# Optimization experiments

Hardware: AMD Instinct MI355X
Metric: run time of the kernel (lower is better)

The kernel has to match this reference:

```python
import jax, jax.numpy as jnp
import numpy as np

CH = 128
C2 = CH // 2
TEMP = 5.0
RATE = 2  # down conv: k=2,s=2,p=0 ; up: convtranspose k=2,s=2,p=0


def _down(x, w, b):
    # Conv2d(ch, ch, kernel=2, stride=2, pad=0) as a patch contraction
    B, C, H, W = x.shape
    xr = x.reshape(B, C, H // 2, 2, W // 2, 2)
    return jnp.einsum('bcipjq,ocpq->boij', xr, w) + b[None, :, None, None]


def _conv1x1(x, w):
    # w: [out, in]
    return jnp.einsum('bchw,oc->bohw', x, w)


def _maxpool2(x):
    B, C, H, W = x.shape
    return x.reshape(B, C, H // 2, 2, W // 2, 2).max(axis=(3, 5))


def _up(x, w, b):
    # ConvTranspose2d(ch, ch, kernel=2, stride=2, pad=0): each pixel -> 2x2 block
    # w: [in, out, 2, 2] (PyTorch layout)
    B, C, H, W = x.shape
    y = jnp.einsum('bchw,copq->bohpwq', x, w).reshape(B, w.shape[1], H * 2, W * 2)
    return y + b[None, :, None, None]


def setup_inputs() -> dict:
    key = jax.random.key(0)
    ks = jax.random.split(key, 12)
    B, H, W = 4, 192, 192
    sc = 0.05
    return {
        'input_x': jax.random.normal(ks[0], (B, CH, H, W), jnp.float32),
        'input_y': jax.random.normal(ks[1], (B, CH, H, W), jnp.float32),
        'down0_w': jax.random.normal(ks[2], (CH, CH, 2, 2), jnp.float32) * sc,
        'down0_b': jax.random.normal(ks[3], (CH,), jnp.float32) * sc,
        'down1_w': jax.random.normal(ks[4], (CH, CH, 2, 2), jnp.float32) * sc,
        'down1_b': jax.random.normal(ks[5], (CH,), jnp.float32) * sc,
        'theta_w': jax.random.normal(ks[6], (C2, CH), jnp.float32) * sc,
        'phi_w': jax.random.normal(ks[7], (C2, CH), jnp.float32) * sc,
        'g_w': jax.random.normal(ks[8], (C2, CH), jnp.float32) * sc,
        'o_w': jax.random.normal(ks[9], (CH, C2), jnp.float32) * sc,
        'up_w': jax.random.normal(ks[10], (CH, CH, 2, 2), jnp.float32) * sc,
        'up_b': jax.random.normal(ks[11], (CH,), jnp.float32) * sc,
        'gamma': jnp.float32(0.5),
    }


def reference(input_x, input_y, down0_w, down0_b, down1_w, down1_b,
              theta_w, phi_w, g_w, o_w, up_w, up_b, gamma):
    x = _down(input_x, down0_w, down0_b)          # [B, CH, h, w]
    y = _down(input_y, down1_w, down1_b)
    B, _, h, w = x.shape
    N = h * w
    M = N // 4

    theta = _conv1x1(x, theta_w).reshape(B, C2, N)          # queries
    phi = _maxpool2(_conv1x1(x, phi_w)).reshape(B, C2, M)   # keys (pooled)
    g = _maxpool2(_conv1x1(y, g_w)).reshape(B, C2, M)       # values (pooled)

    scores = jnp.einsum('bcn,bcm->bnm', theta, phi)          # [B, N, M]
    beta = jax.nn.softmax(TEMP * scores, axis=-1)

    o_map = jnp.einsum('bcm,bnm->bcn', g, beta).reshape(B, C2, h, w)
    o = _conv1x1(o_map, o_w)                                 # [B, CH, h, w]
    out = _up(o, up_w, up_b) + gamma * input_y
    return out
```

## Files before the change

### kernel.cpp

```cpp
#include <hip/hip_runtime.h>
#include <hip/hip_bf16.h>

#define NN    9216
#define MM    2304
#define HW    36864
#define SLABF 4718592
#define TEMPF 5.0f

#define OFF_X   0
#define OFF_Y   4718592
#define OFF_TH  9437184
#define OFF_TP  11796480
#define OFF_PH  14155776
#define OFF_G   14745600
#define OFF_OM  15335424

typedef unsigned short u16;
typedef unsigned int   u32;
typedef __attribute__((ext_vector_type(8))) short bf16x8;
typedef __attribute__((ext_vector_type(4))) float f32x4;

__device__ __forceinline__ u16 f2bf(float f){
  u32 u; __builtin_memcpy(&u,&f,4);
  u32 lsb = (u>>16)&1u; u += 0x7fffu + lsb;
  return (u16)(u>>16);
}
__device__ __forceinline__ u32 pkbf(float a, float b){
  union { __hip_bfloat162 h; u32 u; } v;
  v.h = __float22bfloat162_rn(make_float2(a,b));
  return v.u;
}

__global__ __launch_bounds__(256) void k_down(const float* __restrict__ in,
    const float* __restrict__ w, const float* __restrict__ bias, float* __restrict__ out)
{
  __shared__ __align__(16) float xs[2][6144];
  int blk = blockIdx.x;
  int jt = blk & 1;
  int r1 = blk >> 1;
  int i  = r1 % 96; int b = r1 / 96;
  int t  = threadIdx.x;

  const float* src = in + (size_t)b*128*HW + (size_t)(2*i)*192 + jt*96;

  int cl[3], qq[3];
  #pragma unroll
  for (int k = 0; k < 3; k++) {
    int idx = t + k*256;
    cl[k] = idx / 24;
    qq[k] = idx - cl[k]*24;
  }

  float4 va[3], vb[3];
  #pragma unroll
  for (int k = 0; k < 3; k++) {
    const float* p = src + (size_t)cl[k]*HW + qq[k]*4;
    va[k] = *(const float4*)p;
    vb[k] = *(const float4*)(p + 192);
  }
  #pragma unroll
  for (int k = 0; k < 3; k++) {
    float* d = &xs[0][cl[k]*192 + qq[k]*8];
    *(float4*)d       = make_float4(va[k].x, vb[k].x, va[k].y, vb[k].y);
    *(float4*)(d + 4) = make_float4(va[k].z, vb[k].z, va[k].w, vb[k].w);
  }

  int og = t >> 4, jg = t & 15;
  int o0 = og * 8;
  float acc[8][3];
  #pragma unroll
  for (int oo = 0; oo < 8; oo++)
    #pragma unroll
    for (int jj = 0; jj < 3; jj++) acc[oo][jj] = 0.f;

  const float* wbase = w + (size_t)o0*512;

  for (int ch = 0; ch < 4; ch++) {
    if (ch < 3) {
      #pragma unroll
      for (int k = 0; k < 3; k++) {
        const float* p = src + (size_t)((ch+1)*32 + cl[k])*HW + qq[k]*4;
        va[k] = *(const float4*)p;
        vb[k] = *(const float4*)(p + 192);
      }
    }
    __syncthreads();

    const float* xb = xs[ch & 1];
    const float* wc = wbase + (ch*32)*4;
    for (int c = 0; c < 32; c++) {
      const float* xp = xb + c*192 + jg*12;
      float4 xv0 = *(const float4*)(xp);
      float4 xv1 = *(const float4*)(xp + 4);
      float4 xv2 = *(const float4*)(xp + 8);
      const float* wp = wc + c*4;
      #pragma unroll
      for (int oo = 0; oo < 8; oo++) {
        float4 wv = *(const float4*)(wp + oo*512);
        acc[oo][0] += xv0.x*wv.x + xv0.z*wv.y + xv0.y*wv.z + xv0.w*wv.w;
        acc[oo][1] += xv1.x*wv.x + xv1.z*wv.y + xv1.y*wv.z + xv1.w*wv.w;
        acc[oo][2] += xv2.x*wv.x + xv2.z*wv.y + xv2.y*wv.z + xv2.w*wv.w;
      }
    }

    if (ch < 3) {
      #pragma unroll
      for (int k = 0; k < 3; k++) {
        float* d = &xs[(ch+1) & 1][cl[k]*192 + qq[k]*8];
        *(float4*)d       = make_float4(va[k].x, vb[k].x, va[k].y, vb[k].y);
        *(float4*)(d + 4) = make_float4(va[k].z, vb[k].z, va[k].w, vb[k].w);
      }
    }
  }

  #pragma unroll
  for (int oo = 0; oo < 8; oo++) {
    int o = o0 + oo;
    float bv = bias[o];
    float* op = out + ((size_t)(b*128 + o))*NN + i*96 + jt*48 + jg*3;
    op[0] = acc[oo][0] + bv;
    op[1] = acc[oo][1] + bv;
    op[2] = acc[oo][2] + bv;
  }
}

__global__ __launch_bounds__(256) void k_conv(const float* __restrict__ X,
    const float* __restrict__ WG, float* __restrict__ out)
{
  __shared__ __align__(16) float Xs[128*32];
  __shared__ __align__(16) float wt[128*64];
  int b  = blockIdx.x / 288;
  int n0 = (blockIdx.x % 288) * 32;
  int t  = threadIdx.x;
  for (int idx = t; idx < 8192; idx += 256) {
    int c = idx >> 6, cc = idx & 63;
    wt[idx] = WG[cc*128 + c];
  }
  for (int idx = t; idx < 1024; idx += 256) {
    int c = idx >> 3, wq = idx & 7;
    ((float4*)Xs)[idx] = *(const float4*)&X[((size_t)(b*128 + c))*NN + n0 + wq*4];
  }
  __syncthreads();
  int n = t & 31, og = t >> 5;
  float acc[8];
  #pragma unroll
  for (int k = 0; k < 8; k++) acc[k] = 0.f;
  for (int c = 0; c < 128; c++) {
    float xv = Xs[(c<<5) + n];
    const float* wrow = wt + (c<<6) + og*8;
    float4 wa = *(const float4*)wrow;
    float4 wb = *(const float4*)(wrow + 4);
    acc[0]+=wa.x*xv; acc[1]+=wa.y*xv; acc[2]+=wa.z*xv; acc[3]+=wa.w*xv;
    acc[4]+=wb.x*xv; acc[5]+=wb.y*xv; acc[6]+=wb.z*xv; acc[7]+=wb.w*xv;
  }
  #pragma unroll
  for (int k = 0; k < 8; k++)
    out[((size_t)(b*64 + og*8 + k))*NN + n0 + n] = acc[k];
}

__global__ __launch_bounds__(256) void k_pool(const float* __restrict__ in, float* __restrict__ out)
{
  int t = blockIdx.x*256 + threadIdx.x;
  int J = t % 48; int r = t/48; int I = r % 48; r /= 48; int cc = r & 63; int b = r >> 6;
  const float* p = in + ((size_t)(b*64+cc))*NN + (size_t)(2*I)*96 + 2*J;
  float m = fmaxf(fmaxf(p[0],p[1]), fmaxf(p[96],p[97]));
  out[((size_t)(b*64+cc))*MM + I*48 + J] = m;
}

__global__ __launch_bounds__(256) void k_attn(const float* __restrict__ TH,
    const float* __restrict__ PH, const float* __restrict__ G, float* __restrict__ OUT)
{
  __shared__ __align__(16) u16 sm[13824];
  int t = threadIdx.x;
  int lane = t & 63, wv = t >> 6;
  int quad = lane >> 4, l15 = lane & 15;
  int b  = blockIdx.x / 144;
  int q0 = (blockIdx.x % 144) * 64;
  int qw = q0 + wv*16;

  bf16x8 afrag[2];
  #pragma unroll
  for (int h = 0; h < 2; h++)
    #pragma unroll
    for (int j = 0; j < 8; j++) {
      float v = TEMPF * TH[((size_t)(b*64 + h*32 + quad*8 + j))*NN + qw + l15];
      afrag[h][j] = (short)f2bf(v);
    }

  f32x4 oacc[4];
  #pragma unroll
  for (int ct = 0; ct < 4; ct++)
    #pragma unroll
    for (int r = 0; r < 4; r++) oacc[ct][r] = 0.f;
  float m_r[4], l_r[4];
  #pragma unroll
  for (int r = 0; r < 4; r++) { m_r[r] = -3.0e38f; l_r[r] = 0.f; }

  int kth = t & 63;
  int cg  = t >> 6;

  for (int k0 = 0; k0 < MM; k0 += 64) {
    __syncthreads();
    #pragma unroll
    for (int h = 0; h < 2; h++) {
      int c0 = cg*16 + h*8;
      u32 pk[4];
      #pragma unroll
      for (int p = 0; p < 4; p++) {
        float f0 = PH[((size_t)(b*64 + c0 + 2*p    ))*MM + k0 + kth];
        float f1 = PH[((size_t)(b*64 + c0 + 2*p + 1))*MM + k0 + kth];
        pk[p] = pkbf(f0, f1);
      }
      *(uint4*)&sm[kth*72 + c0] = make_uint4(pk[0],pk[1],pk[2],pk[3]);
    }
    {
      int cc = t >> 2, kq = (t & 3) << 4;
      const float* gp = &G[((size_t)(b*64 + cc))*MM + k0 + kq];
      u32 w[8];
      #pragma unroll
      for (int p = 0; p < 8; p++) w[p] = pkbf(gp[2*p], gp[2*p+1]);
      *(uint4*)&sm[4608 + cc*72 + kq]     = make_uint4(w[0],w[1],w[2],w[3]);
      *(uint4*)&sm[4608 + cc*72 + kq + 8] = make_uint4(w[4],w[5],w[6],w[7]);
    }
    __syncthreads();

    f32x4 s[4];
    #pragma unroll
    for (int kt = 0; kt < 4; kt++) {
      f32x4 acc;
      #pragma unroll
      for (int r = 0; r < 4; r++) acc[r] = 0.f;
      #pragma unroll
      for (int h = 0; h < 2; h++) {
        bf16x8 bfrag = *(const bf16x8*)&sm[(kt*16 + l15)*72 + h*32 + quad*8];
        acc = __builtin_amdgcn_mfma_f32_16x16x32_bf16(afrag[h], bfrag, acc, 0, 0, 0);
      }
      s[kt] = acc;
    }

    float al[4];
    #pragma unroll
    for (int r = 0; r < 4; r++) {
      float mx = fmaxf(fmaxf(s[0][r], s[1][r]), fmaxf(s[2][r], s[3][r]));
      #pragma unroll
      for (int d = 1; d < 16; d <<= 1) mx = fmaxf(mx, __shfl_xor(mx, d));
      float mn = fmaxf(m_r[r], mx);
      float a  = __expf(m_r[r] - mn);
      m_r[r] = mn;
      float ps = 0.f;
      #pragma unroll
      for (int kt = 0; kt < 4; kt++) {
        float p = __expf(s[kt][r] - mn);
        s[kt][r] = p; ps += p;
      }
      #pragma unroll
      for (int d = 1; d < 16; d <<= 1) ps += __shfl_xor(ps, d);
      l_r[r] = l_r[r]*a + ps;
      al[r] = a;
    }
    #pragma unroll
    for (int kt = 0; kt < 4; kt++)
      #pragma unroll
      for (int r = 0; r < 4; r++)
        sm[9216 + wv*1152 + (quad*4 + r)*72 + kt*16 + l15] = f2bf(s[kt][r]);
    #pragma unroll
    for (int ct = 0; ct < 4; ct++)
      #pragma unroll
      for (int r = 0; r < 4; r++) oacc[ct][r] *= al[r];

    bf16x8 pf[2];
    #pragma unroll
    for (int h = 0; h < 2; h++)
      pf[h] = *(const bf16x8*)&sm[9216 + wv*1152 + l15*72 + h*32 + quad*8];
    #pragma unroll
    for (int ct = 0; ct < 4; ct++)
      #pragma unroll
      for (int h = 0; h < 2; h++) {
        bf16x8 gf = *(const bf16x8*)&sm[4608 + (ct*16 + l15)*72 + h*32 + quad*8];
        oacc[ct] = __builtin_amdgcn_mfma_f32_16x16x32_bf16(pf[h], gf, oacc[ct], 0, 0, 0);
      }
  }

  __syncthreads();
  float inv[4];
  #pragma unroll
  for (int r = 0; r < 4; r++) inv[r] = 1.0f / l_r[r];
  float* ol = (float*)sm + wv*1280;
  #pragma unroll
  for (int ct = 0; ct < 4; ct++)
    #pragma unroll
    for (int r = 0; r < 4; r++)
      ol[(ct*16 + l15)*20 + quad*4 + r] = oacc[ct][r] * inv[r];
  __syncthreads();
  const float* orow = ol + lane*20;
  float4 v0 = *(const float4*)(orow);
  float4 v1 = *(const float4*)(orow + 4);
  float4 v2 = *(const float4*)(orow + 8);
  float4 v3 = *(const float4*)(orow + 12);
  float* dst = &OUT[((size_t)(b*64 + lane))*NN + qw];
  *(float4*)(dst)      = v0;
  *(float4*)(dst + 4)  = v1;
  *(float4*)(dst + 8)  = v2;
  *(float4*)(dst + 12) = v3;
}

__global__ __launch_bounds__(256) void k_oconv(const float* __restrict__ X,
    const float* __restrict__ OW, float* __restrict__ dout)
{
  __shared__ __align__(16) float Xs[64*64];
  __shared__ __align__(16) float wt[64*128];
  int b  = blockIdx.x / 144;
  int n0 = (blockIdx.x % 144) * 64;
  int t  = threadIdx.x;
  for (int idx = t; idx < 8192; idx += 256) {
    int cc = idx >> 7, o = idx & 127;
    wt[idx] = OW[o*64 + cc];
  }
  for (int idx = t; idx < 1024; idx += 256) {
    int cc = idx >> 4, wq = idx & 15;
    ((float4*)Xs)[idx] = *(const float4*)&X[((size_t)(b*64 + cc))*NN + n0 + wq*4];
  }
  __syncthreads();
  int n = t & 63, og = t >> 6;
  float acc[32];
  #pragma unroll
  for (int k = 0; k < 32; k++) acc[k] = 0.f;
  for (int cc = 0; cc < 64; cc++) {
    float xv = Xs[(cc << 6) + n];
    const float* wrow = wt + (cc << 7) + og*32;
    #pragma unroll
    for (int k = 0; k < 32; k++) acc[k] += wrow[k]*xv;
  }
  int ng = n0 + n;
  int i = ng / 96, j = ng - (ng/96)*96;
  #pragma unroll
  for (int k = 0; k < 32; k++) {
    int o = og*32 + k;
    size_t addr = (size_t)b*SLABF + (size_t)(o>>2)*HW
                + (size_t)(2*i + ((o>>1)&1))*192 + 2*j + (o&1);
    dout[addr] = acc[k];
  }
}

__global__ __launch_bounds__(256) void k_up(float* __restrict__ dout,
    const float* __restrict__ upw, const float* __restrict__ upb,
    const float* __restrict__ Y, const float* __restrict__ gamma_p)
{
  __shared__ __align__(16) float o_s[128*48];
  int blk = blockIdx.x;
  int jh = blk & 1;
  int r1 = blk >> 1;
  int i = r1 % 96, b = r1 / 96;
  int t = threadIdx.x;
  size_t slab = (size_t)b*SLABF;
  const float* src = dout + slab + (size_t)(2*i)*192 + jh*96;

  for (int idx = t; idx < 6144; idx += 256) {
    int run = idx / 192, rem = idx - run*192;
    int r = rem / 96, cl = rem - r*96;
    float v = src[(size_t)run*HW + r*192 + cl];
    int o = 4*run + 2*r + (cl&1);
    o_s[o*48 + (cl>>1)] = v;
  }
  __syncthreads();

  int op_l = t & 31, jg = t >> 5;
  float gm = *gamma_p;

  for (int oc = 0; oc < 4; oc++) {
    int op = oc*32 + op_l;
    float a0[12], a1[12];
    #pragma unroll
    for (int k = 0; k < 12; k++) { a0[k] = 0.f; a1[k] = 0.f; }

    const float* wp = upw + (size_t)op*4;
    const float* xb = o_s + jg*6;
    for (int c = 0; c < 128; c++) {
      float4 wv = *(const float4*)(wp + (size_t)c*512);
      const float* xp = xb + c*48;
      float2 x01 = *(const float2*)(xp);
      float2 x23 = *(const float2*)(xp + 2);
      float2 x45 = *(const float2*)(xp + 4);
      a0[0] += x01.x*wv.x; a0[1] += x01.x*wv.y; a1[0] += x01.x*wv.z; a1[1] += x01.x*wv.w;
      a0[2] += x01.y*wv.x; a0[3] += x01.y*wv.y; a1[2] += x01.y*wv.z; a1[3] += x01.y*wv.w;
      a0[4] += x23.x*wv.x; a0[5] += x23.x*wv.y; a1[4] += x23.x*wv.z; a1[5] += x23.x*wv.w;
      a0[6] += x23.y*wv.x; a0[7] += x23.y*wv.y; a1[6] += x23.y*wv.z; a1[7] += x23.y*wv.w;
      a0[8] += x45.x*wv.x; a0[9] += x45.x*wv.y; a1[8] += x45.x*wv.z; a1[9] += x45.x*wv.w;
      a0[10]+= x45.y*wv.x; a0[11]+= x45.y*wv.y; a1[10]+= x45.y*wv.z; a1[11]+= x45.y*wv.w;
    }

    float bias = upb[op];
    size_t obase = slab + (size_t)op*HW + (size_t)(2*i)*192 + jh*96 + jg*12;
    float* p0 = dout + obase;
    float* p1 = p0 + 192;
    const float* y0 = Y + obase;
    const float* y1 = y0 + 192;
    #pragma unroll
    for (int q = 0; q < 3; q++) {
      float4 ya = *(const float4*)(y0 + 4*q);
      float4 yb = *(const float4*)(y1 + 4*q);
      *(float4*)(p0 + 4*q) = make_float4(a0[4*q+0]+bias+gm*ya.x, a0[4*q+1]+bias+gm*ya.y,
                                         a0[4*q+2]+bias+gm*ya.z, a0[4*q+3]+bias+gm*ya.w);
      *(float4*)(p1 + 4*q) = make_float4(a1[4*q+0]+bias+gm*yb.x, a1[4*q+1]+bias+gm*yb.y,
                                         a1[4*q+2]+bias+gm*yb.z, a1[4*q+3]+bias+gm*yb.w);
    }
  }
}

extern "C" void kernel_launch(void* const* d_in, const int* in_sizes, int n_in,
                              void* d_out, int out_size, void* d_ws, size_t ws_size,
                              hipStream_t stream) {
  const float* x_in  = (const float*)d_in[0];
  const float* y_in  = (const float*)d_in[1];
  const float* d0w   = (const float*)d_in[2];
  const float* d0b   = (const float*)d_in[3];
  const float* d1w   = (const float*)d_in[4];
  const float* d1b   = (const float*)d_in[5];
  const float* thw   = (const float*)d_in[6];
  const float* phw   = (const float*)d_in[7];
  const float* gw    = (const float*)d_in[8];
  const float* ow    = (const float*)d_in[9];
  const float* upw   = (const float*)d_in[10];
  const float* upb   = (const float*)d_in[11];
  const float* gamma = (const float*)d_in[12];
  float* out = (float*)d_out;

  k_down <<<768,  256, 0, stream>>>(x_in, d0w, d0b, out + OFF_X);
  k_down <<<768,  256, 0, stream>>>(y_in, d1w, d1b, out + OFF_Y);
  k_conv <<<1152, 256, 0, stream>>>(out + OFF_X, thw, out + OFF_TH);
  k_conv <<<1152, 256, 0, stream>>>(out + OFF_X, phw, out + OFF_TP);
  k_pool <<<2304, 256, 0, stream>>>(out + OFF_TP, out + OFF_PH);
  k_conv <<<1152, 256, 0, stream>>>(out + OFF_Y, gw, out + OFF_TP);
  k_pool <<<2304, 256, 0, stream>>>(out + OFF_TP, out + OFF_G);
  k_attn <<<576,  256, 0, stream>>>(out + OFF_TH, out + OFF_PH, out + OFF_G, out + OFF_OM);
  k_oconv<<<576,  256, 0, stream>>>(out + OFF_OM, ow, out);
  k_up   <<<768,  256, 0, stream>>>(out, upw, upb, y_in, gamma);
}
```

Before: 720.1 us.

## Split attention over two key halves with merge kernel and pre-converted bf16 keys/values

New measurement: 687.5 us. 4.5% less time.

```diff
diff --git a/kernel.cpp b/kernel.cpp
--- a/kernel.cpp
+++ b/kernel.cpp
@@ -14,6 +14,8 @@
 #define OFF_PH  14155776
 #define OFF_G   14745600
 #define OFF_OM  15335424
+#define POSZ    2359296
+#define MLSZ    73728
 
 typedef unsigned short u16;
 typedef unsigned int   u32;
@@ -158,25 +160,58 @@
     out[((size_t)(b*64 + og*8 + k))*NN + n0 + n] = acc[k];
 }
 
-__global__ __launch_bounds__(256) void k_pool(const float* __restrict__ in, float* __restrict__ out)
+__global__ __launch_bounds__(256) void k_poolT(const float* __restrict__ in, u16* __restrict__ out)
+{
+  __shared__ float ps[48*68];
+  int blk = blockIdx.x;
+  int I = blk % 48, b = blk / 48;
+  int t = threadIdx.x;
+  int cc = t >> 2, jq = t & 3;
+  const float* base = in + ((size_t)(b*64 + cc))*NN + (size_t)(2*I)*96;
+  #pragma unroll
+  for (int j = 0; j < 12; j++) {
+    int J = jq*12 + j;
+    const float* p = base + 2*J;
+    float2 a = *(const float2*)p;
+    float2 c = *(const float2*)(p + 96);
+    ps[J*68 + cc] = fmaxf(fmaxf(a.x, a.y), fmaxf(c.x, c.y));
+  }
+  __syncthreads();
+  u32* op = (u32*)out + ((size_t)b*2304 + I*48)*32;
+  for (int idx = t; idx < 1536; idx += 256) {
+    int row = idx >> 5, pr = idx & 31;
+    op[row*32 + pr] = pkbf(ps[row*68 + 2*pr], ps[row*68 + 2*pr + 1]);
+  }
+}
+
+__global__ __launch_bounds__(256) void k_poolB(const float* __restrict__ in, u16* __restrict__ out)
 {
   int t = blockIdx.x*256 + threadIdx.x;
-  int J = t % 48; int r = t/48; int I = r % 48; r /= 48; int cc = r & 63; int b = r >> 6;
-  const float* p = in + ((size_t)(b*64+cc))*NN + (size_t)(2*I)*96 + 2*J;
-  float m = fmaxf(fmaxf(p[0],p[1]), fmaxf(p[96],p[97]));
-  out[((size_t)(b*64+cc))*MM + I*48 + J] = m;
+  int pr = t % 24; int r = t / 24;
+  int I = r % 48; r /= 48;
+  int cc = r & 63, b = r >> 6;
+  const float* p = in + ((size_t)(b*64 + cc))*NN + (size_t)(2*I)*96 + 4*pr;
+  float4 r0 = *(const float4*)p;
+  float4 r1 = *(const float4*)(p + 96);
+  float m0 = fmaxf(fmaxf(r0.x, r0.y), fmaxf(r1.x, r1.y));
+  float m1 = fmaxf(fmaxf(r0.z, r0.w), fmaxf(r1.z, r1.w));
+  ((u32*)out)[((size_t)(b*64 + cc))*1152 + I*24 + pr] = pkbf(m0, m1);
 }
 
 __global__ __launch_bounds__(256) void k_attn(const float* __restrict__ TH,
-    const float* __restrict__ PH, const float* __restrict__ G, float* __restrict__ OUT)
+    const u16* __restrict__ PHT, const u16* __restrict__ GB,
+    float* __restrict__ PO, float* __restrict__ ML)
 {
   __shared__ __align__(16) u16 sm[13824];
   int t = threadIdx.x;
   int lane = t & 63, wv = t >> 6;
   int quad = lane >> 4, l15 = lane & 15;
-  int b  = blockIdx.x / 144;
-  int q0 = (blockIdx.x % 144) * 64;
-  int qw = q0 + wv*16;
+  int id = blockIdx.x;
+  int b   = id / 288;
+  int rem = id % 288;
+  int ks  = rem / 144;
+  int q0  = (rem % 144) * 64;
+  int qw  = q0 + wv*16;
 
   bf16x8 afrag[2];
   #pragma unroll
@@ -196,31 +231,22 @@
   #pragma unroll
   for (int r = 0; r < 4; r++) { m_r[r] = -3.0e38f; l_r[r] = 0.f; }
 
-  int kth = t & 63;
-  int cg  = t >> 6;
-
-  for (int k0 = 0; k0 < MM; k0 += 64) {
+  int k0end = ks*1152 + 1152;
+  for (int k0 = ks*1152; k0 < k0end; k0 += 64) {
     __syncthreads();
     #pragma unroll
-    for (int h = 0; h < 2; h++) {
-      int c0 = cg*16 + h*8;
-      u32 pk[4];
-      #pragma unroll
-      for (int p = 0; p < 4; p++) {
-        float f0 = PH[((size_t)(b*64 + c0 + 2*p    ))*MM + k0 + kth];
-        float f1 = PH[((size_t)(b*64 + c0 + 2*p + 1))*MM + k0 + kth];
-        pk[p] = pkbf(f0, f1);
-      }
-      *(uint4*)&sm[kth*72 + c0] = make_uint4(pk[0],pk[1],pk[2],pk[3]);
-    }
-    {
-      int cc = t >> 2, kq = (t & 3) << 4;
-      const float* gp = &G[((size_t)(b*64 + cc))*MM + k0 + kq];
-      u32 w[8];
-      #pragma unroll
-      for (int p = 0; p < 8; p++) w[p] = pkbf(gp[2*p], gp[2*p+1]);
-      *(uint4*)&sm[4608 + cc*72 + kq]     = make_uint4(w[0],w[1],w[2],w[3]);
-      *(uint4*)&sm[4608 + cc*72 + kq + 8] = make_uint4(w[4],w[5],w[6],w[7]);
+    for (int s = 0; s < 2; s++) {
+      int idx = t + s*256;
+      int row = idx >> 3, q = idx & 7;
+      uint4 v = ((const uint4*)(PHT + ((size_t)(b*2304 + k0 + row))*64))[q];
+      *(uint4*)&sm[row*72 + q*8] = v;
+    }
+    #pragma unroll
+    for (int s = 0; s < 2; s++) {
+      int idx = t + s*256;
+      int row = idx >> 3, q = idx & 7;
+      uint4 v = *(const uint4*)(GB + (size_t)(b*64 + row)*2304 + k0 + q*8);
+      *(uint4*)&sm[4608 + row*72 + q*8] = v;
     }
     __syncthreads();
 
@@ -282,26 +308,67 @@
   }
 
   __syncthreads();
-  float inv[4];
-  #pragma unroll
-  for (int r = 0; r < 4; r++) inv[r] = 1.0f / l_r[r];
+  if (l15 == 0) {
+    #pragma unroll
+    for (int r = 0; r < 4; r++) {
+      int qg = qw + quad*4 + r;
+      ML[(size_t)(ks*4 + b)*9216 + qg]         = m_r[r];
+      ML[MLSZ + (size_t)(ks*4 + b)*9216 + qg]  = l_r[r];
+    }
+  }
   float* ol = (float*)sm + wv*1280;
   #pragma unroll
   for (int ct = 0; ct < 4; ct++)
     #pragma unroll
     for (int r = 0; r < 4; r++)
-      ol[(ct*16 + l15)*20 + quad*4 + r] = oacc[ct][r] * inv[r];
+      ol[(ct*16 + l15)*20 + quad*4 + r] = oacc[ct][r];
   __syncthreads();
   const float* orow = ol + lane*20;
   float4 v0 = *(const float4*)(orow);
   float4 v1 = *(const float4*)(orow + 4);
   float4 v2 = *(const float4*)(orow + 8);
   float4 v3 = *(const float4*)(orow + 12);
-  float* dst = &OUT[((size_t)(b*64 + lane))*NN + qw];
+  float* dst = PO + (size_t)ks*POSZ + ((size_t)(b*64 + lane))*NN + qw;
   *(float4*)(dst)      = v0;
   *(float4*)(dst + 4)  = v1;
   *(float4*)(dst + 8)  = v2;
   *(float4*)(dst + 12) = v3;
+}
+
+__global__ __launch_bounds__(256) void k_amerge(const float* __restrict__ PO,
+    const float* __restrict__ ML, float* __restrict__ OUT)
+{
+  int idx = blockIdx.x*256 + threadIdx.x;
+  size_t flat = (size_t)idx*4;
+  int bc = (int)(flat / NN);
+  int n  = (int)(flat - (size_t)bc*NN);
+  int b  = bc >> 6;
+  float4 p0 = *(const float4*)&PO[flat];
+  float4 p1 = *(const float4*)&PO[POSZ + flat];
+  const float* m0p = ML + (size_t)b*9216 + n;
+  const float* m1p = ML + (size_t)(4 + b)*9216 + n;
+  const float* l0p = ML + MLSZ + (size_t)b*9216 + n;
+  const float* l1p = ML + MLSZ + (size_t)(4 + b)*9216 + n;
+  float4 m0 = *(const float4*)m0p, m1 = *(const float4*)m1p;
+  float4 l0 = *(const float4*)l0p, l1 = *(const float4*)l1p;
+  float4 r;
+  {
+    float M = fmaxf(m0.x, m1.x); float a0 = __expf(m0.x - M), a1 = __expf(m1.x - M);
+    r.x = (a0*p0.x + a1*p1.x) / (a0*l0.x + a1*l1.x);
+  }
+  {
+    float M = fmaxf(m0.y, m1.y); float a0 = __expf(m0.y - M), a1 = __expf(m1.y - M);
+    r.y = (a0*p0.y + a1*p1.y) / (a0*l0.y + a1*l1.y);
+  }
+  {
+    float M = fmaxf(m0.z, m1.z); float a0 = __expf(m0.z - M), a1 = __expf(m1.z - M);
+    r.z = (a0*p0.z + a1*p1.z) / (a0*l0.z + a1*l1.z);
+  }
+  {
+    float M = fmaxf(m0.w, m1.w); float a0 = __expf(m0.w - M), a1 = __expf(m1.w - M);
+    r.w = (a0*p0.w + a1*p1.w) / (a0*l0.w + a1*l1.w);
+  }
+  *(float4*)&OUT[flat] = r;
 }
 
 __global__ __launch_bounds__(256) void k_oconv(const float* __restrict__ X,
@@ -425,14 +492,16 @@
   const float* gamma = (const float*)d_in[12];
   float* out = (float*)d_out;
 
-  k_down <<<768,  256, 0, stream>>>(x_in, d0w, d0b, out + OFF_X);
-  k_down <<<768,  256, 0, stream>>>(y_in, d1w, d1b, out + OFF_Y);
-  k_conv <<<1152, 256, 0, stream>>>(out + OFF_X, thw, out + OFF_TH);
-  k_conv <<<1152, 256, 0, stream>>>(out + OFF_X, phw, out + OFF_TP);
-  k_pool <<<2304, 256, 0, stream>>>(out + OFF_TP, out + OFF_PH);
-  k_conv <<<1152, 256, 0, stream>>>(out + OFF_Y, gw, out + OFF_TP);
-  k_pool <<<2304, 256, 0, stream>>>(out + OFF_TP, out + OFF_G);
-  k_attn <<<576,  256, 0, stream>>>(out + OFF_TH, out + OFF_PH, out + OFF_G, out + OFF_OM);
-  k_oconv<<<576,  256, 0, stream>>>(out + OFF_OM, ow, out);
-  k_up   <<<768,  256, 0, stream>>>(out, upw, upb, y_in, gamma);
-}
+  k_down  <<<768,  256, 0, stream>>>(x_in, d0w, d0b, out + OFF_X);
+  k_down  <<<768,  256, 0, stream>>>(y_in, d1w, d1b, out + OFF_Y);
+  k_conv  <<<1152, 256, 0, stream>>>(out + OFF_X, thw, out + OFF_TH);
+  k_conv  <<<1152, 256, 0, stream>>>(out + OFF_X, phw, out + OFF_TP);
+  k_poolT <<<192,  256, 0, stream>>>(out + OFF_TP, (u16*)(out + OFF_PH));
+  k_conv  <<<1152, 256, 0, stream>>>(out + OFF_Y, gw, out + OFF_TP);
+  k_poolB <<<1152, 256, 0, stream>>>(out + OFF_TP, (u16*)(out + OFF_G));
+  k_attn  <<<1152, 256, 0, stream>>>(out + OFF_TH, (const u16*)(out + OFF_PH),
+                                     (const u16*)(out + OFF_G), out + OFF_X, out + OFF_Y);
+  k_amerge<<<2304, 256, 0, stream>>>(out + OFF_X, out + OFF_Y, out + OFF_OM);
+  k_oconv <<<576,  256, 0, stream>>>(out + OFF_OM, ow, out);
+  k_up    <<<768,  256, 0, stream>>>(out, upw, upb, y_in, gamma);
+}
```
